# Kernel optimization log

Hardware: AMD Instinct MI355X
Metric: run time of the kernel (lower is better)

## Reference

```python
import jax, jax.numpy as jnp
import numpy as np

BLOCK = 128          # fp8 quantization block size (from linear_deepseek_v3)
FP8_MAX = 448.0      # max representable value of float8_e4m3fn
F8 = jnp.float8_e4m3fn
G, T, K, N = 8, 1024, 7168, 2048


def setup_inputs() -> dict:
    key = jax.random.key(0)
    kx, kw, kb = jax.random.split(key, 3)
    xs = jax.random.normal(kx, (G, T, K), jnp.float32)
    # Build an fp8 block-quantized weight + per-(128x128)-block fp32 scale,
    # matching the stored self.weight (fp8) and self.scale parameters.
    w_raw = jax.random.normal(kw, (G, N, K), jnp.float32)
    wb = w_raw.reshape(G, N // BLOCK, BLOCK, K // BLOCK, BLOCK)
    amax = jnp.max(jnp.abs(wb), axis=(2, 4))            # [G, NB, KB]
    scale = amax / FP8_MAX
    w_q = (wb / scale[:, :, None, :, None]).astype(F8).astype(jnp.float32)
    weight = w_q.reshape(G, N, K)                        # fp8 code values held in fp32
    bias = jax.random.normal(kb, (G, N), jnp.float32) * 0.02
    return {"xs": xs, "weight": weight, "scale": scale, "bias": bias}


def reference(xs, weight, scale, bias):
    """Grouped fp8 block-quantized GEMM with inline dequant.
    xs:     [G, T, K] fp32 activations (one slab per group)
    weight: [G, N, K] fp8-quantized weights (stored as fp32 code values)
    scale:  [G, N/128, K/128] fp32 per-block weight scales
    bias:   [G, N] fp32
    """
    g, t, k = xs.shape
    n = weight.shape[1]
    kb, nb = k // BLOCK, n // BLOCK
    # --- act_quant_deepseek_v3: per (token, 128-col block) absmax/448 scale ---
    xb = xs.reshape(g, t, kb, BLOCK)
    a_scale = jnp.max(jnp.abs(xb), axis=-1) / FP8_MAX        # [G, T, KB]
    x_q = (xb / a_scale[..., None]).astype(F8).astype(jnp.float32)
    x_deq = (x_q * a_scale[..., None]).reshape(g, t, k)      # fused dequant
    # --- weight dequant: broadcast per-(128x128)-block scale ---
    w_deq = (weight.reshape(g, nb, BLOCK, kb, BLOCK)
             * scale[:, :, None, :, None]).reshape(g, n, k)
    # --- grouped GEMM (y = x A^T) + bias, fp32 accumulation ---
    y = jnp.einsum('gtk,gnk->gtn', x_deq, w_deq) + bias[:, None, :]
    return y
```

## Files before the change

kernel.cpp:

```cpp
#include <hip/hip_runtime.h>
#include <hip/hip_bf16.h>
#include <stdint.h>

#define G_ 8
#define T_ 1024
#define K_ 7168
#define N_ 2048
#define KB_ (K_/128)
#define NB_ (N_/128)
#define NT_ (K_/64)

typedef __attribute__((ext_vector_type(4))) float f32x4;
typedef __attribute__((ext_vector_type(2))) float f32x2;
typedef __attribute__((ext_vector_type(8))) short bf16x8;

typedef __attribute__((address_space(3))) uint32_t lds_u32_t;
typedef const __attribute__((address_space(1))) uint32_t gbl_u32_t;

__device__ __forceinline__ void gload_lds16(const void* gsrc, const void* ldst)
{
    __builtin_amdgcn_global_load_lds(
        (gbl_u32_t*)(uintptr_t)gsrc,
        (lds_u32_t*)(uint32_t)(uintptr_t)ldst, 16, 0, 0);
}

__device__ __forceinline__ void blockbar()
{
    asm volatile("" ::: "memory");
    __builtin_amdgcn_s_barrier();
    asm volatile("" ::: "memory");
}

__global__ __launch_bounds__(256) void act_quant_kernel(
    const float* __restrict__ xs, __hip_bfloat16* __restrict__ xq)
{
    const int grp = (blockIdx.x * 256 + threadIdx.x) >> 5;
    const int l   = threadIdx.x & 31;
    const size_t base = (size_t)grp * 128 + (size_t)l * 4;

    const float4 v = *(const float4*)(xs + base);
    float am = fmaxf(fmaxf(fabsf(v.x), fabsf(v.y)), fmaxf(fabsf(v.z), fabsf(v.w)));
#pragma unroll
    for (int off = 1; off <= 16; off <<= 1)
        am = fmaxf(am, __shfl_xor(am, off, 64));
    const float s = am / 448.0f;

    const int pk01 = __builtin_amdgcn_cvt_pk_fp8_f32(v.x / s, v.y / s, 0, false);
    const int pk23 = __builtin_amdgcn_cvt_pk_fp8_f32(v.z / s, v.w / s, 0, false);
    const f32x2 d01 = __builtin_amdgcn_cvt_pk_f32_fp8(pk01, false);
    const f32x2 d23 = __builtin_amdgcn_cvt_pk_f32_fp8(pk23, false);

    union { uint2 u; __hip_bfloat16 h[4]; } p;
    p.h[0] = __float2bfloat16(d01[0] * s);
    p.h[1] = __float2bfloat16(d01[1] * s);
    p.h[2] = __float2bfloat16(d23[0] * s);
    p.h[3] = __float2bfloat16(d23[1] * s);
    *(uint2*)(xq + base) = p.u;
}

#define MFMA_Q(MH, NH)                                                        \
  { _Pragma("unroll") for (int m = 0; m < 4; ++m) {                           \
      _Pragma("unroll") for (int n = 0; n < 2; ++n) {                         \
        _Pragma("unroll") for (int ks = 0; ks < 2; ++ks) {                    \
          acc[(MH)*4+m][(NH)*2+n] = __builtin_amdgcn_mfma_f32_16x16x32_bf16(  \
              bA[m*2+ks], bB[((NH)*2+n)*2+ks], acc[(MH)*4+m][(NH)*2+n],       \
              0, 0, 0);                                                       \
  } } } }

#define LDA(m, ks, MH, b)                                                     \
  bA[(m)*2+(ks)] = *(const bf16x8*)(smem + (b)*32768 +                        \
      (wrow + (MH)*64 + (m)*16 + l15)*128 + colK[ks])

#define LDB(n, ks, b)                                                         \
  bB[(n)*2+(ks)] = *(const bf16x8*)(smem + 65536 + (b)*32768 +                \
      (wcol + (n)*16 + l15)*128 + colK[ks])

#define STG_A(c, t, b) gload_lds16(pA[c] + (size_t)(t)*64,                    \
      smem + (b)*32768 + (c)*8192 + dstw)

#define LOAD_B(t)                                                             \
  { _Pragma("unroll") for (int c = 0; c < 4; ++c) {                           \
      const float* s_ = pW[c] + (size_t)(t) * 64;                             \
      br[c*2]   = *(const f32x4*)(s_);                                        \
      br[c*2+1] = *(const f32x4*)(s_ + 4);                                    \
  } }

#define WRITE_B(t, b)                                                         \
  { const int kb_ = (t) >> 1;                                                 \
    const float s0_ = scale[scb + kb_];                                       \
    const float s1_ = scale[scb + KB_ + kb_];                                 \
    _Pragma("unroll") for (int c = 0; c < 4; ++c) {                           \
      const float sc_ = (c < 2) ? s0_ : s1_;                                  \
      union { __hip_bfloat16 h[8]; bf16x8 v; } u_;                            \
      _Pragma("unroll") for (int e = 0; e < 4; ++e) {                         \
        u_.h[e]     = __float2bfloat16(br[c*2][e]   * sc_);                   \
        u_.h[e + 4] = __float2bfloat16(br[c*2+1][e] * sc_);                   \
      }                                                                       \
      *(bf16x8*)(smem + 65536 + (b)*32768 + (c*64 + brow)*128 + bslot) = u_.v;\
  } }

__global__ __launch_bounds__(512) void gemm8_kernel(
    const __hip_bfloat16* __restrict__ xq, const float* __restrict__ w,
    const float* __restrict__ scale, const float* __restrict__ bias,
    float* __restrict__ y)
{
    __shared__ char smem[131072];

    const int bx0 = blockIdx.x;
    const int bx  = (bx0 & 7) * 32 + (bx0 >> 3);
    const int g   = bx >> 5;
    const int tm  = (bx >> 3) & 3;
    const int tn  = bx & 7;
    const int t0  = tm * 256, n0 = tn * 256;

    const int tid = threadIdx.x, lane = tid & 63, wid = tid >> 6;
    const int l15 = lane & 15, lhi = lane >> 4;
    const int wrow = (wid >> 2) * 128;
    const int wcol = (wid & 3) * 64;

    const __hip_bfloat16* Ag = xq + (size_t)g * T_ * K_;
    const float*          Wg = w  + (size_t)g * N_ * K_;

    const int srow = tid >> 3;
    const int xoff = ((tid & 7) ^ (srow & 7)) * 8;
    const __hip_bfloat16* pA[4];
#pragma unroll
    for (int c = 0; c < 4; ++c)
        pA[c] = Ag + (size_t)(t0 + c * 64 + srow) * K_ + xoff;
    const int dstw = wid * 1024;

    const int brow  = tid >> 3;
    const int gslot = tid & 7;
    const int bslot = (gslot ^ (brow & 7)) * 16;
    const float* pW[4];
#pragma unroll
    for (int c = 0; c < 4; ++c)
        pW[c] = Wg + (size_t)(n0 + c * 64 + brow) * K_ + gslot * 8;
    const int scb = ((size_t)g * NB_ + tn * 2) * KB_;

    const int rxor = (l15 & 7) << 4;
    int colK[2];
    colK[0] = (lhi * 16) ^ rxor;
    colK[1] = (64 + lhi * 16) ^ rxor;

    f32x4 acc[8][4] = {};
    bf16x8 bA[8], bB[8];
    f32x4 br[8];

    LOAD_B(0);
#pragma unroll
    for (int c = 0; c < 4; ++c) STG_A(c, 0, 0);
    asm volatile("s_waitcnt vmcnt(4)" ::: "memory");
    WRITE_B(0, 0);
    LOAD_B(1);
#pragma unroll
    for (int c = 0; c < 4; ++c) STG_A(c, 1, 1);
    asm volatile("s_waitcnt vmcnt(4)" ::: "memory");
    WRITE_B(1, 1);
    asm volatile("s_waitcnt vmcnt(0) lgkmcnt(0)" ::: "memory");
    blockbar();

    for (int u = 0; u < NT_; ++u) {
        const int cb = u & 1;
        const bool pf = (u + 2 < NT_);

        if (pf) LOAD_B(u + 2);
        LDA(0,0,0,cb); LDA(0,1,0,cb); LDA(1,0,0,cb); LDA(1,1,0,cb);
        LDA(2,0,0,cb); LDA(2,1,0,cb); LDA(3,0,0,cb); LDA(3,1,0,cb);
        LDB(0,0,cb);   LDB(0,1,cb);   LDB(1,0,cb);   LDB(1,1,cb);
        blockbar();
        asm volatile("s_waitcnt lgkmcnt(0)" ::: "memory");
        __builtin_amdgcn_s_setprio(1);
        MFMA_Q(0, 0);
        __builtin_amdgcn_s_setprio(0);
        blockbar();

        LDB(2,0,cb); LDB(2,1,cb); LDB(3,0,cb); LDB(3,1,cb);
        if (pf) { STG_A(0, u+2, cb); STG_A(2, u+2, cb); }
        blockbar();
        asm volatile("s_waitcnt lgkmcnt(0)" ::: "memory");
        __builtin_amdgcn_s_setprio(1);
        MFMA_Q(0, 1);
        __builtin_amdgcn_s_setprio(0);
        blockbar();

        LDA(0,0,1,cb); LDA(0,1,1,cb); LDA(1,0,1,cb); LDA(1,1,1,cb);
        LDA(2,0,1,cb); LDA(2,1,1,cb); LDA(3,0,1,cb); LDA(3,1,1,cb);
        if (pf) { STG_A(1, u+2, cb); STG_A(3, u+2, cb); }
        blockbar();
        asm volatile("s_waitcnt lgkmcnt(0)" ::: "memory");
        __builtin_amdgcn_s_setprio(1);
        MFMA_Q(1, 0);
        __builtin_amdgcn_s_setprio(0);
        blockbar();

        if (pf) {
            asm volatile("s_waitcnt vmcnt(4)" ::: "memory");
            WRITE_B(u + 2, cb);
        } else if (u + 1 < NT_) {
            asm volatile("s_waitcnt vmcnt(0)" ::: "memory");
        }
        __builtin_amdgcn_s_setprio(1);
        MFMA_Q(1, 1);
        __builtin_amdgcn_s_setprio(0);
        blockbar();
    }

    float* Yg = y + (size_t)g * T_ * N_;
#pragma unroll
    for (int n = 0; n < 4; ++n) {
        const int col = n0 + wcol + n * 16 + l15;
        const float bv = bias[g * N_ + col];
#pragma unroll
        for (int m = 0; m < 8; ++m) {
            const int r0 = t0 + wrow + m * 16 + lhi * 4;
#pragma unroll
            for (int j = 0; j < 4; ++j)
                Yg[(size_t)(r0 + j) * N_ + col] = acc[m][n][j] + bv;
        }
    }
}

extern "C" void kernel_launch(void* const* d_in, const int* in_sizes, int n_in,
                              void* d_out, int out_size, void* d_ws, size_t ws_size,
                              hipStream_t stream)
{
    const float* xs     = (const float*)d_in[0];
    const float* weight = (const float*)d_in[1];
    const float* scale  = (const float*)d_in[2];
    const float* bias   = (const float*)d_in[3];
    float* y = (float*)d_out;

    __hip_bfloat16* xq = (__hip_bfloat16*)d_ws;

    act_quant_kernel<<<(G_ * T_ * KB_) / 8, 256, 0, stream>>>(xs, xq);
    gemm8_kernel<<<256, 512, 0, stream>>>(xq, weight, scale, bias, y);
}
```

Baseline: 385.1 us.

## Switch GEMM to native fp8 MFMA with per-block scales applied to accumulators

Activations are now stored as fp8 bytes plus per-(token,128-block) scales, and weights are re-encoded from fp32 code values to fp8 bytes in a separate kernel. The GEMM uses the 16x16x128 f8f6f4 scaled MFMA with unit scales, then multiplies each block result by activation scale times weight scale before accumulating in fp32. This halves or quarters the bytes streamed per K tile and removes the in-loop fp32-to-bf16 weight dequant, but adds a full weight recode pass every call and extra per-tile FMA work for scaling.

```diff
diff --git a/kernel.cpp b/kernel.cpp
--- a/kernel.cpp
+++ b/kernel.cpp
@@ -8,11 +8,10 @@
 #define N_ 2048
 #define KB_ (K_/128)
 #define NB_ (N_/128)
-#define NT_ (K_/64)
+#define NT8_ 56
 
 typedef __attribute__((ext_vector_type(4))) float f32x4;
-typedef __attribute__((ext_vector_type(2))) float f32x2;
-typedef __attribute__((ext_vector_type(8))) short bf16x8;
+typedef __attribute__((ext_vector_type(8))) int   i32x8;
 
 typedef __attribute__((address_space(3))) uint32_t lds_u32_t;
 typedef const __attribute__((address_space(1))) uint32_t gbl_u32_t;
@@ -32,7 +31,8 @@
 }
 
 __global__ __launch_bounds__(256) void act_quant_kernel(
-    const float* __restrict__ xs, __hip_bfloat16* __restrict__ xq)
+    const float* __restrict__ xs, uint8_t* __restrict__ xq8,
+    float* __restrict__ ascale)
 {
     const int grp = (blockIdx.x * 256 + threadIdx.x) >> 5;
     const int l   = threadIdx.x & 31;
@@ -45,66 +45,80 @@
         am = fmaxf(am, __shfl_xor(am, off, 64));
     const float s = am / 448.0f;
 
-    const int pk01 = __builtin_amdgcn_cvt_pk_fp8_f32(v.x / s, v.y / s, 0, false);
-    const int pk23 = __builtin_amdgcn_cvt_pk_fp8_f32(v.z / s, v.w / s, 0, false);
-    const f32x2 d01 = __builtin_amdgcn_cvt_pk_f32_fp8(pk01, false);
-    const f32x2 d23 = __builtin_amdgcn_cvt_pk_f32_fp8(pk23, false);
-
-    union { uint2 u; __hip_bfloat16 h[4]; } p;
-    p.h[0] = __float2bfloat16(d01[0] * s);
-    p.h[1] = __float2bfloat16(d01[1] * s);
-    p.h[2] = __float2bfloat16(d23[0] * s);
-    p.h[3] = __float2bfloat16(d23[1] * s);
-    *(uint2*)(xq + base) = p.u;
-}
-
-#define MFMA_Q(MH, NH)                                                        \
+    int pk = __builtin_amdgcn_cvt_pk_fp8_f32(v.x / s, v.y / s, 0, false);
+    pk     = __builtin_amdgcn_cvt_pk_fp8_f32(v.z / s, v.w / s, pk, true);
+    *(uint32_t*)(xq8 + base) = (uint32_t)pk;
+
+    if (l == 0) {
+        const int kb = grp % KB_;
+        const int t  = (grp / KB_) & (T_ - 1);
+        const int g  = grp / (KB_ * T_);
+        ascale[(((size_t)(g * 4 + (t >> 8))) * KB_ + kb) * 256 + (t & 255)] = s;
+    }
+}
+
+__global__ __launch_bounds__(256) void wrecode_kernel(
+    const float* __restrict__ w, uint8_t* __restrict__ wq8)
+{
+    const size_t i = ((size_t)blockIdx.x * 256 + threadIdx.x) * 16;
+    uint32_t o[4];
+#pragma unroll
+    for (int q = 0; q < 4; ++q) {
+        const float4 a = *(const float4*)(w + i + q * 4);
+        int pk = __builtin_amdgcn_cvt_pk_fp8_f32(a.x, a.y, 0, false);
+        pk     = __builtin_amdgcn_cvt_pk_fp8_f32(a.z, a.w, pk, true);
+        o[q] = (uint32_t)pk;
+    }
+    *(uint4*)(wq8 + i) = make_uint4(o[0], o[1], o[2], o[3]);
+}
+
+union Frag { i32x8 v; struct { int4 lo, hi; } p; };
+
+#define RD_A(mh)                                                              \
+  { _Pragma("unroll") for (int m = 0; m < 4; ++m) {                           \
+      const int r  = wrow + ((mh)*4 + m)*16 + l15;                            \
+      const int rx = (r & 7) << 4;                                            \
+      const char* bp = smem + cb*32768 + r*128;                               \
+      aF[m].p.lo = *(const int4*)(bp + ((lhi*32) ^ rx));                      \
+      aF[m].p.hi = *(const int4*)(bp + ((lhi*32 + 16) ^ rx));                 \
+      const float4 sv = *(const float4*)(smem + 131072 + ((u>>3)&1)*8192 +    \
+          (u & 7)*1024 + (wrow + ((mh)*4 + m)*16 + lhi*4)*4);                 \
+      asw[m][0] = sv.x*wsc; asw[m][1] = sv.y*wsc;                             \
+      asw[m][2] = sv.z*wsc; asw[m][3] = sv.w*wsc;                             \
+  } }
+
+#define RD_B(nh)                                                              \
+  { _Pragma("unroll") for (int n = 0; n < 2; ++n) {                           \
+      const int r  = wcol + ((nh)*2 + n)*16 + l15;                            \
+      const int rx = (r & 7) << 4;                                            \
+      const char* bp = smem + 65536 + cb*32768 + r*128;                       \
+      bF[(nh)*2+n].p.lo = *(const int4*)(bp + ((lhi*32) ^ rx));               \
+      bF[(nh)*2+n].p.hi = *(const int4*)(bp + ((lhi*32 + 16) ^ rx));          \
+  } }
+
+#define MM(mh, nh)                                                            \
   { _Pragma("unroll") for (int m = 0; m < 4; ++m) {                           \
       _Pragma("unroll") for (int n = 0; n < 2; ++n) {                         \
-        _Pragma("unroll") for (int ks = 0; ks < 2; ++ks) {                    \
-          acc[(MH)*4+m][(NH)*2+n] = __builtin_amdgcn_mfma_f32_16x16x32_bf16(  \
-              bA[m*2+ks], bB[((NH)*2+n)*2+ks], acc[(MH)*4+m][(NH)*2+n],       \
-              0, 0, 0);                                                       \
-  } } } }
-
-#define LDA(m, ks, MH, b)                                                     \
-  bA[(m)*2+(ks)] = *(const bf16x8*)(smem + (b)*32768 +                        \
-      (wrow + (MH)*64 + (m)*16 + l15)*128 + colK[ks])
-
-#define LDB(n, ks, b)                                                         \
-  bB[(n)*2+(ks)] = *(const bf16x8*)(smem + 65536 + (b)*32768 +                \
-      (wcol + (n)*16 + l15)*128 + colK[ks])
-
-#define STG_A(c, t, b) gload_lds16(pA[c] + (size_t)(t)*64,                    \
-      smem + (b)*32768 + (c)*8192 + dstw)
-
-#define LOAD_B(t)                                                             \
-  { _Pragma("unroll") for (int c = 0; c < 4; ++c) {                           \
-      const float* s_ = pW[c] + (size_t)(t) * 64;                             \
-      br[c*2]   = *(const f32x4*)(s_);                                        \
-      br[c*2+1] = *(const f32x4*)(s_ + 4);                                    \
-  } }
-
-#define WRITE_B(t, b)                                                         \
-  { const int kb_ = (t) >> 1;                                                 \
-    const float s0_ = scale[scb + kb_];                                       \
-    const float s1_ = scale[scb + KB_ + kb_];                                 \
-    _Pragma("unroll") for (int c = 0; c < 4; ++c) {                           \
-      const float sc_ = (c < 2) ? s0_ : s1_;                                  \
-      union { __hip_bfloat16 h[8]; bf16x8 v; } u_;                            \
-      _Pragma("unroll") for (int e = 0; e < 4; ++e) {                         \
-        u_.h[e]     = __float2bfloat16(br[c*2][e]   * sc_);                   \
-        u_.h[e + 4] = __float2bfloat16(br[c*2+1][e] * sc_);                   \
-      }                                                                       \
-      *(bf16x8*)(smem + 65536 + (b)*32768 + (c*64 + brow)*128 + bslot) = u_.v;\
-  } }
-
-__global__ __launch_bounds__(512) void gemm8_kernel(
-    const __hip_bfloat16* __restrict__ xq, const float* __restrict__ w,
-    const float* __restrict__ scale, const float* __restrict__ bias,
-    float* __restrict__ y)
-{
-    __shared__ char smem[131072];
+        f32x4 blk = __builtin_amdgcn_mfma_scale_f32_16x16x128_f8f6f4(         \
+            aF[m].v, bF[(nh)*2+n].v, z4, 0, 0,                                \
+            0, 0x7F7F7F7F, 0, 0x7F7F7F7F);                                    \
+        _Pragma("unroll") for (int j = 0; j < 4; ++j)                         \
+          acc[(mh)*4+m][(nh)*2+n][j] += blk[j] * asw[m][j];                   \
+  } } }
+
+#define STG_A8(c, t, b) gload_lds16(pA8[c] + (size_t)(t)*128,                 \
+      smem + (b)*32768 + (c)*8192 + tid*16)
+#define STG_B8(c, t, b) gload_lds16(pB8[c] + (size_t)(t)*128,                 \
+      smem + 65536 + (b)*32768 + (c)*8192 + tid*16)
+#define STG_S(c) gload_lds16(pS + (size_t)(c)*2048,                           \
+      smem + 131072 + ((c)&1)*8192 + tid*16)
+
+__global__ __launch_bounds__(512) void gemm_fp8_kernel(
+    const uint8_t* __restrict__ xq8, const uint8_t* __restrict__ wq8,
+    const float* __restrict__ ascale, const float* __restrict__ wscale,
+    const float* __restrict__ bias, float* __restrict__ y)
+{
+    __shared__ char smem[147456];
 
     const int bx0 = blockIdx.x;
     const int bx  = (bx0 & 7) * 32 + (bx0 >> 3);
@@ -118,91 +132,73 @@
     const int wrow = (wid >> 2) * 128;
     const int wcol = (wid & 3) * 64;
 
-    const __hip_bfloat16* Ag = xq + (size_t)g * T_ * K_;
-    const float*          Wg = w  + (size_t)g * N_ * K_;
+    const uint8_t* Ag = xq8 + (size_t)g * T_ * K_;
+    const uint8_t* Bg = wq8 + (size_t)g * N_ * K_;
 
     const int srow = tid >> 3;
-    const int xoff = ((tid & 7) ^ (srow & 7)) * 8;
-    const __hip_bfloat16* pA[4];
-#pragma unroll
-    for (int c = 0; c < 4; ++c)
-        pA[c] = Ag + (size_t)(t0 + c * 64 + srow) * K_ + xoff;
-    const int dstw = wid * 1024;
-
-    const int brow  = tid >> 3;
-    const int gslot = tid & 7;
-    const int bslot = (gslot ^ (brow & 7)) * 16;
-    const float* pW[4];
-#pragma unroll
-    for (int c = 0; c < 4; ++c)
-        pW[c] = Wg + (size_t)(n0 + c * 64 + brow) * K_ + gslot * 8;
-    const int scb = ((size_t)g * NB_ + tn * 2) * KB_;
-
-    const int rxor = (l15 & 7) << 4;
-    int colK[2];
-    colK[0] = (lhi * 16) ^ rxor;
-    colK[1] = (64 + lhi * 16) ^ rxor;
-
+    const int xoff = ((tid & 7) ^ (srow & 7)) * 16;
+    const uint8_t* pA8[4];
+    const uint8_t* pB8[4];
+#pragma unroll
+    for (int c = 0; c < 4; ++c) {
+        pA8[c] = Ag + (size_t)(t0 + c * 64 + srow) * K_ + xoff;
+        pB8[c] = Bg + (size_t)(n0 + c * 64 + srow) * K_ + xoff;
+    }
+    const float* pS = ascale + ((size_t)(g * 4 + tm) * KB_) * 256 + tid * 4;
+    const int wscb = (g * NB_ + ((n0 + wcol) >> 7)) * KB_;
+
+    const f32x4 z4 = {0.f, 0.f, 0.f, 0.f};
     f32x4 acc[8][4] = {};
-    bf16x8 bA[8], bB[8];
-    f32x4 br[8];
-
-    LOAD_B(0);
-#pragma unroll
-    for (int c = 0; c < 4; ++c) STG_A(c, 0, 0);
-    asm volatile("s_waitcnt vmcnt(4)" ::: "memory");
-    WRITE_B(0, 0);
-    LOAD_B(1);
-#pragma unroll
-    for (int c = 0; c < 4; ++c) STG_A(c, 1, 1);
-    asm volatile("s_waitcnt vmcnt(4)" ::: "memory");
-    WRITE_B(1, 1);
-    asm volatile("s_waitcnt vmcnt(0) lgkmcnt(0)" ::: "memory");
+    Frag aF[4], bF[4];
+    float asw[4][4];
+
+    STG_S(0);
+#pragma unroll
+    for (int c = 0; c < 4; ++c) { STG_A8(c, 0, 0); STG_B8(c, 0, 0); }
+#pragma unroll
+    for (int c = 0; c < 4; ++c) { STG_A8(c, 1, 1); STG_B8(c, 1, 1); }
+    asm volatile("s_waitcnt vmcnt(8)" ::: "memory");
     blockbar();
 
-    for (int u = 0; u < NT_; ++u) {
+    for (int u = 0; u < NT8_; ++u) {
         const int cb = u & 1;
-        const bool pf = (u + 2 < NT_);
-
-        if (pf) LOAD_B(u + 2);
-        LDA(0,0,0,cb); LDA(0,1,0,cb); LDA(1,0,0,cb); LDA(1,1,0,cb);
-        LDA(2,0,0,cb); LDA(2,1,0,cb); LDA(3,0,0,cb); LDA(3,1,0,cb);
-        LDB(0,0,cb);   LDB(0,1,cb);   LDB(1,0,cb);   LDB(1,1,cb);
+        const bool pf = (u + 2 < NT8_);
+        const float wsc = wscale[wscb + u];
+
+        if ((u & 7) == 0 && u + 8 < NT8_) STG_S((u >> 3) + 1);
+        RD_A(0); RD_B(0);
         blockbar();
         asm volatile("s_waitcnt lgkmcnt(0)" ::: "memory");
         __builtin_amdgcn_s_setprio(1);
-        MFMA_Q(0, 0);
-        __builtin_amdgcn_s_setprio(0);
-        blockbar();
-
-        LDB(2,0,cb); LDB(2,1,cb); LDB(3,0,cb); LDB(3,1,cb);
-        if (pf) { STG_A(0, u+2, cb); STG_A(2, u+2, cb); }
+        MM(0, 0);
+        __builtin_amdgcn_s_setprio(0);
+        blockbar();
+
+        RD_B(1);
+        if (pf) { STG_A8(0, u + 2, cb); STG_A8(2, u + 2, cb); }
         blockbar();
         asm volatile("s_waitcnt lgkmcnt(0)" ::: "memory");
         __builtin_amdgcn_s_setprio(1);
-        MFMA_Q(0, 1);
-        __builtin_amdgcn_s_setprio(0);
-        blockbar();
-
-        LDA(0,0,1,cb); LDA(0,1,1,cb); LDA(1,0,1,cb); LDA(1,1,1,cb);
-        LDA(2,0,1,cb); LDA(2,1,1,cb); LDA(3,0,1,cb); LDA(3,1,1,cb);
-        if (pf) { STG_A(1, u+2, cb); STG_A(3, u+2, cb); }
+        MM(0, 1);
+        __builtin_amdgcn_s_setprio(0);
+        blockbar();
+
+        RD_A(1);
+        if (pf) { STG_B8(0, u + 2, cb); STG_B8(1, u + 2, cb); }
         blockbar();
         asm volatile("s_waitcnt lgkmcnt(0)" ::: "memory");
         __builtin_amdgcn_s_setprio(1);
-        MFMA_Q(1, 0);
-        __builtin_amdgcn_s_setprio(0);
-        blockbar();
-
-        if (pf) {
-            asm volatile("s_waitcnt vmcnt(4)" ::: "memory");
-            WRITE_B(u + 2, cb);
-        } else if (u + 1 < NT_) {
-            asm volatile("s_waitcnt vmcnt(0)" ::: "memory");
-        }
-        __builtin_amdgcn_s_setprio(1);
-        MFMA_Q(1, 1);
-        __builtin_amdgcn_s_setprio(0);
+        MM(1, 0);
+        __builtin_amdgcn_s_setprio(0);
+        blockbar();
+
+        if (pf) { STG_A8(1, u + 2, cb); STG_A8(3, u + 2, cb);
+                  STG_B8(2, u + 2, cb); STG_B8(3, u + 2, cb); }
+        __builtin_amdgcn_s_setprio(1);
+        MM(1, 1);
+        __builtin_amdgcn_s_setprio(0);
+        if (pf)                  asm volatile("s_waitcnt vmcnt(8)" ::: "memory");
+        else if (u + 1 < NT8_)   asm volatile("s_waitcnt vmcnt(0)" ::: "memory");
         blockbar();
     }
 
@@ -231,8 +227,14 @@
     const float* bias   = (const float*)d_in[3];
     float* y = (float*)d_out;
 
-    __hip_bfloat16* xq = (__hip_bfloat16*)d_ws;
-
-    act_quant_kernel<<<(G_ * T_ * KB_) / 8, 256, 0, stream>>>(xs, xq);
-    gemm8_kernel<<<256, 512, 0, stream>>>(xq, weight, scale, bias, y);
-}
+    uint8_t* xq8   = (uint8_t*)d_ws;
+    float*   ascl  = (float*)((char*)d_ws + 58720256);
+    uint8_t* wq8   = (uint8_t*)((char*)d_ws + 60555264);
+
+    act_quant_kernel<<<(G_ * T_ * KB_) / 8, 256, 0, stream>>>(xs, xq8, ascl);
+
+    wrecode_kernel<<<(int)(((size_t)G_ * N_ * K_ / 16) / 256), 256, 0, stream>>>(
+        weight, wq8);
+
+    gemm_fp8_kernel<<<256, 512, 0, stream>>>(xq8, wq8, ascl, scale, bias, y);
+}
```

Measured after the change: 373.2 us. 3.1% less time.
